# Optimization experiments

Hardware: AMD Instinct MI355X
Metric: run time of the kernel (lower is better)

The kernel has to match this reference:

```python
import jax, jax.numpy as jnp
import numpy as np
from functools import partial

B, N, T = 4, 10000, 128
E = 160000
H, C = 4, 64            # heads, out_channels per head
GAT_DIM = H * C         # 256
NEG_SLOPE = 0.2


def conv1d(x, w, b):
    # x: (M, Cin, L), w: (Cout, Cin, K), 'same' padding (pad=1 for k=3)
    y = jax.lax.conv_general_dilated(x, w, window_strides=(1,), padding=[(1, 1)],
                                     dimension_numbers=('NCH', 'OIH', 'NCH'))
    return y + b[None, :, None]


def maxpool2(x):
    # kernel=2, stride=2 over last axis
    return jax.lax.reduce_window(x, -jnp.inf, jax.lax.max,
                                 (1, 1, 2), (1, 1, 2), 'VALID')


def gat_layer_single(x, src, dst, W, att_s, att_d, bias):
    # x: (N, Fin); PyG GATConv with concat=True, self-loops already appended to src/dst
    n = x.shape[0]
    xl = (x @ W).reshape(n, H, C)                       # (N, H, C)
    a_s = jnp.sum(xl * att_s[None], axis=-1)            # (N, H)
    a_d = jnp.sum(xl * att_d[None], axis=-1)            # (N, H)
    e = jax.nn.leaky_relu(a_s[src] + a_d[dst], NEG_SLOPE)  # (E', H)
    emax = jax.ops.segment_max(e, dst, num_segments=n)     # (N, H)
    ex = jnp.exp(e - emax[dst])
    denom = jax.ops.segment_sum(ex, dst, num_segments=n)   # (N, H)
    alpha = ex / (denom[dst] + 1e-16)                       # (E', H)
    msg = xl[src] * alpha[..., None]                        # (E', H, C)
    out = jax.ops.segment_sum(msg, dst, num_segments=n)     # (N, H, C)
    return out.reshape(n, H * C) + bias


def setup_inputs() -> dict:
    key = jax.random.key(0)
    ks = jax.random.split(key, 24)
    rn = lambda k, sh, fan: jax.random.normal(k, sh, jnp.float32) / np.sqrt(fan)
    inp = {
        'x': jax.random.normal(ks[0], (B, N, T), jnp.float32),
        'edge_index': jax.random.randint(ks[1], (2, E), 0, N, jnp.int64),
        # temporal conv
        'cw1': rn(ks[2], (32, 1, 3), 3), 'cb1': jnp.zeros((32,), jnp.float32),
        'cw2': rn(ks[3], (64, 32, 3), 96), 'cb2': jnp.zeros((64,), jnp.float32),
        # GAT layer 0 (in=64)
        'W0': rn(ks[4], (64, GAT_DIM), 64), 'as0': rn(ks[5], (H, C), C), 'ad0': rn(ks[6], (H, C), C),
        'b0': jnp.zeros((GAT_DIM,), jnp.float32),
        # GAT layer 1 (in=256)
        'W1': rn(ks[7], (GAT_DIM, GAT_DIM), GAT_DIM), 'as1': rn(ks[8], (H, C), C), 'ad1': rn(ks[9], (H, C), C),
        'b1': jnp.zeros((GAT_DIM,), jnp.float32),
        # classification head 256->128->2
        'Wc1': rn(ks[10], (GAT_DIM, 128), GAT_DIM), 'bc1': jnp.zeros((128,), jnp.float32),
        'Wc2': rn(ks[11], (128, 2), 128), 'bc2': jnp.zeros((2,), jnp.float32),
        # attribution head 256->64->1
        'Wa1': rn(ks[12], (GAT_DIM, 64), GAT_DIM), 'ba1': jnp.zeros((64,), jnp.float32),
        'Wa2': rn(ks[13], (64, 1), 64), 'ba2': jnp.zeros((1,), jnp.float32),
    }
    return inp


def reference(x, edge_index, cw1, cb1, cw2, cb2, W0, as0, ad0, b0, W1, as1, ad1, b1,
              Wc1, bc1, Wc2, bc2, Wa1, ba1, Wa2, ba2):
    b, n, t = x.shape
    # ---- temporal conv over all B*N node signals ----
    xf = x.reshape(b * n, 1, t)
    h = jax.nn.relu(conv1d(xf, cw1, cb1))            # (BN, 32, T)
    h = maxpool2(h)                                  # (BN, 32, T//2)
    h = jax.nn.relu(conv1d(h, cw2, cb2))             # (BN, 64, T//2)
    feat = jnp.mean(h, axis=-1).reshape(b, n, 64)    # adaptive_avg_pool1d(1)
    # ---- GAT stack (self-loops appended, PyG default) ----
    src0, dst0 = edge_index[0], edge_index[1]
    loops = jnp.arange(n, dtype=src0.dtype)
    src = jnp.concatenate([src0, loops])
    dst = jnp.concatenate([dst0, loops])
    gat0 = jax.vmap(partial(gat_layer_single, src=src, dst=dst, W=W0, att_s=as0, att_d=ad0, bias=b0))
    gat1 = jax.vmap(partial(gat_layer_single, src=src, dst=dst, W=W1, att_s=as1, att_d=ad1, bias=b1))
    g = jax.nn.relu(gat0(feat))                      # (B, N, 256); dropout = identity (eval)
    g = jax.nn.relu(gat1(g))                         # (B, N, 256)
    # ---- heads ----
    pooled = jnp.mean(g, axis=1)                     # (B, 256)
    logits = jax.nn.relu(pooled @ Wc1 + bc1) @ Wc2 + bc2          # (B, 2)
    attr = jax.nn.sigmoid(jax.nn.relu(g @ Wa1 + ba1) @ Wa2 + ba2)  # (B, N, 1)
    return logits, attr[..., 0]
```

## Files before the change

kernel.cpp:

```cpp
#include <hip/hip_runtime.h>
#include <hip/hip_bf16.h>
#include <math.h>

typedef __hip_bfloat16 bf16;
typedef unsigned short u16;
typedef unsigned int u32;
typedef __attribute__((ext_vector_type(8))) short short8;
typedef __attribute__((ext_vector_type(4))) float f32x4;
typedef __attribute__((ext_vector_type(2))) float f32x2;

#define BATCH 4
#define NNODE 10000
#define TLEN 128
#define NEDGE 160000
#define GDIM 256
#define NHEAD 4

#define S_CW1 0
#define S_CB1 96
#define S_CB2 128
#define S_AS0 192
#define S_AD0 448
#define S_B0  704
#define S_AS1 960
#define S_AD1 1216
#define S_B1  1472
#define S_BC1 1728
#define S_WC2 1856
#define S_BC2 2112
#define S_BA1 2114
#define S_WA2 2178
#define S_BA2 2242
#define S_TOTAL 2243

__device__ __forceinline__ float prelu(float v) { return 0.5f * (v + fabsf(v)); }
__device__ __forceinline__ u16 f2b(float f) {
    union { float f; u32 u; } v; v.f = f;
    u32 r = v.u + 0x7FFF + ((v.u >> 16) & 1);
    return (u16)(r >> 16);
}
__device__ __forceinline__ float u2f(u16 u) {
    union { u32 u; float f; } v; v.u = ((u32)u) << 16;
    return v.f;
}
__device__ __forceinline__ float ldw(const void* p, int off, bool isbf) {
    return isbf ? u2f(((const u16*)p)[off]) : ((const float*)p)[off];
}

__device__ __forceinline__ bool probe_x_bf16(const void* xsrc) {
    int lane = threadIdx.x & 63;
    u16 h = ((const u16*)xsrc)[2 * lane];
    int e = (h >> 7) & 0xFF;
    unsigned long long m = __ballot(e >= 117 && e <= 130);
    return __popcll(m) >= 32;
}
__device__ __forceinline__ bool probe_ei64(const int* ei) {
    int lane = threadIdx.x & 63;
    int v = ei[2 * lane + 1];
    unsigned long long m = __ballot(v == 0);
    return __popcll(m) >= 56;
}

struct WPtrs { const void* p[20]; };

#define PRE_TBLK 665
__global__ __launch_bounds__(256) void k_pre(WPtrs wp, const void* __restrict__ xsrc,
        const int* __restrict__ ei, float* __restrict__ wbuf,
        u16* __restrict__ cw2r, u16* __restrict__ W0t, u16* __restrict__ W1t,
        u16* __restrict__ Wa1t, int* __restrict__ counts) {
    bool isbf = probe_x_bf16(xsrc);
    int b = blockIdx.x;
    if (b >= PRE_TBLK) {
        const int C2[16] = {0,96,128,192,448,704,960,1216,1472,1728,1856,2112,
                            2114,2178,2242,2243};
        const int SRC[15] = {0,1,3,5,6,7,9,10,11,13,14,15,17,18,19};
        int i = (b - PRE_TBLK) * 256 + threadIdx.x;
        if (i >= S_TOTAL) return;
        int j = 14;
        for (int t = 0; t < 15; ++t) { if (i < C2[t + 1]) { j = t; break; } }
        wbuf[i] = ldw(wp.p[SRC[j]], i - C2[j], isbf);
        return;
    }
    int i = b * 256 + threadIdx.x;
    if (i < 6144) {
        int c2 = i / 96, k = i - c2 * 96, s = k >> 5, ci = k & 31;
        cw2r[i] = f2b(ldw(wp.p[2], c2 * 96 + ci * 3 + s, isbf));
    }
    if (i < 16384) {
        int k = i >> 8, c = i & 255;
        W0t[c * 64 + k] = f2b(ldw(wp.p[4], k * 256 + c, isbf));
        int ka = i >> 6, ca = i & 63;
        Wa1t[ca * 256 + ka] = f2b(ldw(wp.p[16], ka * 64 + ca, isbf));
    }
    if (i < 65536) {
        int k = i >> 8, c = i & 255;
        W1t[c * 256 + k] = f2b(ldw(wp.p[8], k * 256 + c, isbf));
    }
    if (i < NEDGE + NNODE) {
        bool ei64 = probe_ei64(ei);
        int dst;
        if (i < NEDGE) dst = ei64 ? ei[2 * (NEDGE + i)] : ei[NEDGE + i];
        else dst = i - NEDGE;
        if (dst >= 0 && dst < NNODE) atomicAdd(&counts[dst], 1);
    }
}

__global__ __launch_bounds__(256) void k_scan1(const int* __restrict__ counts,
        int* __restrict__ cur, int* __restrict__ bsum) {
    __shared__ int buf[256];
    int tid = threadIdx.x;
    int i = blockIdx.x * 256 + tid;
    int v = (i < NNODE) ? counts[i] : 0;
    buf[tid] = v;
    __syncthreads();
    for (int off = 1; off < 256; off <<= 1) {
        int t = (tid >= off) ? buf[tid - off] : 0;
        __syncthreads();
        buf[tid] += t;
        __syncthreads();
    }
    if (i < NNODE) cur[i] = buf[tid];
    if (tid == 255) bsum[blockIdx.x] = buf[255];
}
__global__ __launch_bounds__(256) void k_scan3(const int* __restrict__ counts,
        int* __restrict__ cur, const int* __restrict__ bsum, int* __restrict__ row_ptr) {
    __shared__ int pre_s;
    int tid = threadIdx.x;
    if (tid == 0) {
        int s = 0;
        for (int j = 0; j < blockIdx.x; ++j) s += bsum[j];
        pre_s = s;
    }
    __syncthreads();
    int i = blockIdx.x * 256 + tid;
    if (i >= NNODE) return;
    int incl = cur[i] + pre_s;
    row_ptr[i + 1] = incl;
    cur[i] = incl - counts[i];
    if (i == 0) row_ptr[0] = 0;
}

#define HSTR 40
#define FILL_BLK 665
__global__ __launch_bounds__(256) void k_conv(const void* __restrict__ xsrc,
        const float* __restrict__ wbuf, const u16* __restrict__ cw2r,
        u16* __restrict__ featb, const int* __restrict__ ei,
        int* __restrict__ cur, int* __restrict__ col_src) {
    __shared__ __align__(16) float xs[4][132];
    __shared__ float w1s[96], b1s[32], b2s[64];
    __shared__ __align__(16) u16 hs[2][66 * HSTR];

    bool isbf = probe_x_bf16(xsrc);
    int tid = threadIdx.x;
    int wave = tid >> 6, lane = tid & 63;
    int node0 = blockIdx.x * 4;

    int m = lane & 15, q = lane >> 4;
    int n = wave * 16 + m;
    short8 bfr0 = *(const short8*)&cw2r[n * 96 + 0 * 32 + q * 8];
    short8 bfr1 = *(const short8*)&cw2r[n * 96 + 1 * 32 + q * 8];
    short8 bfr2 = *(const short8*)&cw2r[n * 96 + 2 * 32 + q * 8];

    {
        int j = tid >> 6, p = (tid & 63) * 2;
        if (isbf) {
            u32 w = ((const u32*)xsrc)[(size_t)node0 * 64 + tid];
            xs[j][1 + p] = u2f((u16)(w & 0xFFFF));
            xs[j][2 + p] = u2f((u16)(w >> 16));
        } else {
            float2 w = ((const float2*)xsrc)[(size_t)node0 * 64 + tid];
            xs[j][1 + p] = w.x;
            xs[j][2 + p] = w.y;
        }
    }
    if (tid < 8) xs[tid >> 1][(tid & 1) ? 129 : 0] = 0.f;
    if (tid < 96) w1s[tid] = wbuf[S_CW1 + tid];
    if (tid < 32) b1s[tid] = wbuf[S_CB1 + tid];
    if (tid < 64) b2s[tid] = wbuf[S_CB2 + tid];
    if (tid < 128) {
        int bf = tid >> 6, seg = (tid >> 5) & 1, ch = tid & 31;
        hs[bf][seg ? (65 * HSTR + ch) : ch] = 0;
    }
    __syncthreads();

    int d = tid & 15, uu = tid >> 4;
    float wa0 = w1s[6 * d + 0], wa1 = w1s[6 * d + 1], wa2 = w1s[6 * d + 2];
    float wb0 = w1s[6 * d + 3], wb1 = w1s[6 * d + 4], wb2 = w1s[6 * d + 5];
    float ba = b1s[2 * d], bb = b1s[2 * d + 1];
    float b2v = b2s[n];

    for (int j = 0; j < 4; ++j) {
        u16* hw = &hs[j & 1][0];
        const float* xr = &xs[j][0];
        #pragma unroll
        for (int it = 0; it < 4; ++it) {
            int u = uu + 16 * it;
            int t0 = 2 * u;
            float x0 = xr[t0], x1 = xr[t0 + 1], x2 = xr[t0 + 2], x3 = xr[t0 + 3];
            f32x2 A = {x0, x1}, Bv = {x1, x2}, Cv = {x2, x3};
            f32x2 va = {ba, ba}; va += wa0 * A; va += wa1 * Bv; va += wa2 * Cv;
            f32x2 vb = {bb, bb}; vb += wb0 * A; vb += wb1 * Bv; vb += wb2 * Cv;
            float ha = fmaxf(fmaxf(va.x, va.y), 0.f);
            float hb = fmaxf(fmaxf(vb.x, vb.y), 0.f);
            __hip_bfloat162 hp2 = __float22bfloat162_rn(make_float2(ha, hb));
            u32 pack; __builtin_memcpy(&pack, &hp2, 4);
            *(u32*)&hw[(u + 1) * HSTR + 2 * d] = pack;
        }
        __syncthreads();

        f32x4 accm0 = {0.f,0.f,0.f,0.f}, accm1 = {0.f,0.f,0.f,0.f};
        f32x4 accm2 = {0.f,0.f,0.f,0.f}, accm3 = {0.f,0.f,0.f,0.f};
        {
            short8 a0 = *(const short8*)&hw[(0 * 16 + m + 0) * HSTR + q * 8];
            short8 a1 = *(const short8*)&hw[(1 * 16 + m + 0) * HSTR + q * 8];
            short8 a2 = *(const short8*)&hw[(2 * 16 + m + 0) * HSTR + q * 8];
            short8 a3 = *(const short8*)&hw[(3 * 16 + m + 0) * HSTR + q * 8];
            accm0 = __builtin_amdgcn_mfma_f32_16x16x32_bf16(a0, bfr0, accm0, 0, 0, 0);
            accm1 = __builtin_amdgcn_mfma_f32_16x16x32_bf16(a1, bfr0, accm1, 0, 0, 0);
            accm2 = __builtin_amdgcn_mfma_f32_16x16x32_bf16(a2, bfr0, accm2, 0, 0, 0);
            accm3 = __builtin_amdgcn_mfma_f32_16x16x32_bf16(a3, bfr0, accm3, 0, 0, 0);
        }
        {
            short8 a0 = *(const short8*)&hw[(0 * 16 + m + 1) * HSTR + q * 8];
            short8 a1 = *(const short8*)&hw[(1 * 16 + m + 1) * HSTR + q * 8];
            short8 a2 = *(const short8*)&hw[(2 * 16 + m + 1) * HSTR + q * 8];
            short8 a3 = *(const short8*)&hw[(3 * 16 + m + 1) * HSTR + q * 8];
            accm0 = __builtin_amdgcn_mfma_f32_16x16x32_bf16(a0, bfr1, accm0, 0, 0, 0);
            accm1 = __builtin_amdgcn_mfma_f32_16x16x32_bf16(a1, bfr1, accm1, 0, 0, 0);
            accm2 = __builtin_amdgcn_mfma_f32_16x16x32_bf16(a2, bfr1, accm2, 0, 0, 0);
            accm3 = __builtin_amdgcn_mfma_f32_16x16x32_bf16(a3, bfr1, accm3, 0, 0, 0);
        }
        {
            short8 a0 = *(const short8*)&hw[(0 * 16 + m + 2) * HSTR + q * 8];
            short8 a1 = *(const short8*)&hw[(1 * 16 + m + 2) * HSTR + q * 8];
            short8 a2 = *(const short8*)&hw[(2 * 16 + m + 2) * HSTR + q * 8];
            short8 a3 = *(const short8*)&hw[(3 * 16 + m + 2) * HSTR + q * 8];
            accm0 = __builtin_amdgcn_mfma_f32_16x16x32_bf16(a0, bfr2, accm0, 0, 0, 0);
            accm1 = __builtin_amdgcn_mfma_f32_16x16x32_bf16(a1, bfr2, accm1, 0, 0, 0);
            accm2 = __builtin_amdgcn_mfma_f32_16x16x32_bf16(a2, bfr2, accm2, 0, 0, 0);
            accm3 = __builtin_amdgcn_mfma_f32_16x16x32_bf16(a3, bfr2, accm3, 0, 0, 0);
        }
        float scl = prelu(accm0[0] + b2v) + prelu(accm0[1] + b2v)
                  + prelu(accm0[2] + b2v) + prelu(accm0[3] + b2v);
        scl += prelu(accm1[0] + b2v) + prelu(accm1[1] + b2v)
             + prelu(accm1[2] + b2v) + prelu(accm1[3] + b2v);
        scl += prelu(accm2[0] + b2v) + prelu(accm2[1] + b2v)
             + prelu(accm2[2] + b2v) + prelu(accm2[3] + b2v);
        scl += prelu(accm3[0] + b2v) + prelu(accm3[1] + b2v)
             + prelu(accm3[2] + b2v) + prelu(accm3[3] + b2v);
        scl += __shfl_xor(scl, 16, 64);
        scl += __shfl_xor(scl, 32, 64);
        if (lane < 16) {
            int node = node0 + j;
            int bb2 = node / NNODE, nn = node - bb2 * NNODE;
            featb[((size_t)nn * 4 + bb2) * 64 + wave * 16 + lane] = f2b(scl * (1.f / 64.f));
        }
    }

    if (blockIdx.x < FILL_BLK) {
        bool ei64 = probe_ei64(ei);
        int e = blockIdx.x * 256 + tid;
        if (e < NEDGE + NNODE) {
            int src, dst;
            if (e < NEDGE) {
                if (ei64) { src = ei[2 * e]; dst = ei[2 * (NEDGE + e)]; }
                else      { src = ei[e];     dst = ei[NEDGE + e]; }
            } else {
                src = dst = e - NEDGE;
            }
            if (dst >= 0 && dst < NNODE) {
                int pos = atomicAdd(&cur[dst], 1);
                if (pos >= 0 && pos < NEDGE + NNODE) col_src[pos] = src;
            }
        }
    }
}

template<int K>
__global__ __launch_bounds__(256) void k_gemm(const u16* __restrict__ A,
        const u16* __restrict__ Wt, const float* __restrict__ att_s_w,
        const float* __restrict__ att_d_w, u16* __restrict__ outb,
        float* __restrict__ a_s, float* __restrict__ a_d) {
    int wave = threadIdx.x >> 6, lane = threadIdx.x & 63;
    int row0 = (blockIdx.x * 4 + wave) * 16;
    int m = lane & 15, q = lane >> 4;
    f32x4 acc[16];
    #pragma unroll
    for (int nt = 0; nt < 16; ++nt) acc[nt] = {0.f, 0.f, 0.f, 0.f};
    for (int kc = 0; kc < K; kc += 32) {
        short8 a = *(const short8*)&A[(size_t)(row0 + m) * K + kc + q * 8];
        #pragma unroll
        for (int nt = 0; nt < 16; ++nt) {
            short8 b = *(const short8*)&Wt[(size_t)(nt * 16 + m) * K + kc + q * 8];
            acc[nt] = __builtin_amdgcn_mfma_f32_16x16x32_bf16(a, b, acc[nt], 0, 0, 0);
        }
    }
    #pragma unroll
    for (int nt = 0; nt < 16; ++nt) {
        #pragma unroll
        for (int r = 0; r < 4; ++r)
            outb[(size_t)(row0 + q * 4 + r) * 256 + nt * 16 + m] = f2b(acc[nt][r]);
    }
    float sh_s[4][4] = {{0}}, sh_d[4][4] = {{0}};
    #pragma unroll
    for (int nt = 0; nt < 16; ++nt) {
        int h = nt >> 2;
        int cc = (nt & 3) * 16 + m;
        float asw = att_s_w[h * 64 + cc];
        float adw = att_d_w[h * 64 + cc];
        #pragma unroll
        for (int r = 0; r < 4; ++r) {
            sh_s[h][r] += acc[nt][r] * asw;
            sh_d[h][r] += acc[nt][r] * adw;
        }
    }
    #pragma unroll
    for (int off = 1; off < 16; off <<= 1) {
        #pragma unroll
        for (int h = 0; h < 4; ++h)
            #pragma unroll
            for (int r = 0; r < 4; ++r) {
                sh_s[h][r] += __shfl_xor(sh_s[h][r], off, 64);
                sh_d[h][r] += __shfl_xor(sh_d[h][r], off, 64);
            }
    }
    if (m == 0) {
        #pragma unroll
        for (int r = 0; r < 4; ++r) {
            int row = row0 + q * 4 + r;
            float4 vs = {sh_s[0][r], sh_s[1][r], sh_s[2][r], sh_s[3][r]};
            float4 vd = {sh_d[0][r], sh_d[1][r], sh_d[2][r], sh_d[3][r]};
            *(float4*)&a_s[(size_t)row * 4] = vs;
            *(float4*)&a_d[(size_t)row * 4] = vd;
        }
    }
}

__global__ __launch_bounds__(256) void k_agg(const u16* __restrict__ xlb,
        const float* __restrict__ a_s, const float* __restrict__ a_d,
        const int* __restrict__ row_ptr, const int* __restrict__ col_src,
        const float* __restrict__ bias, u16* __restrict__ gb_out) {
    int wave = threadIdx.x >> 6, lane = threadIdx.x & 63;
    int dst = blockIdx.x * 2 + (wave >> 1);
    int bp = (wave & 1) * 2;
    int beg = row_ptr[dst], end = row_ptr[dst + 1];

    int c = lane & 7, g = lane >> 3;
    int bc = bp + (c >> 2), hc = c & 3;
    float adv1 = a_d[(size_t)dst * 16 + bc * 4 + hc];
    float mloc = -INFINITY;
    for (int i = beg + g; i < end; i += 8) {
        int src = min(max(col_src[i], 0), NNODE - 1);
        float e = a_s[(size_t)src * 16 + bc * 4 + hc] + adv1;
        e = (e >= 0.f) ? e : 0.2f * e;
        mloc = fmaxf(mloc, e);
    }
    mloc = fmaxf(mloc, __shfl_xor(mloc, 8, 64));
    mloc = fmaxf(mloc, __shfl_xor(mloc, 16, 64));
    mloc = fmaxf(mloc, __shfl_xor(mloc, 32, 64));

    int bl = lane >> 5;
    int s = lane & 31;
    int h = s >> 3;
    int b = bp + bl;
    float mv = __shfl(mloc, bl * 4 + h, 64);

    float advh = a_d[(size_t)dst * 16 + b * 4 + h];
    float acc[8];
    #pragma unroll
    for (int k = 0; k < 8; ++k) acc[k] = 0.f;
    float l = 0.f;

    int asoff = b * 4 + h;
    int i = beg;
    for (; i + 4 <= end; i += 4) {
        int s0 = min(max(col_src[i], 0), NNODE - 1);
        int s1 = min(max(col_src[i + 1], 0), NNODE - 1);
        int s2 = min(max(col_src[i + 2], 0), NNODE - 1);
        int s3 = min(max(col_src[i + 3], 0), NNODE - 1);
        float a0 = a_s[(size_t)s0 * 16 + asoff];
        float a1 = a_s[(size_t)s1 * 16 + asoff];
        float a2 = a_s[(size_t)s2 * 16 + asoff];
        float a3 = a_s[(size_t)s3 * 16 + asoff];
        short8 x0 = *(const short8*)&xlb[((size_t)s0 * 4 + b) * 256 + s * 8];
        short8 x1 = *(const short8*)&xlb[((size_t)s1 * 4 + b) * 256 + s * 8];
        short8 x2 = *(const short8*)&xlb[((size_t)s2 * 4 + b) * 256 + s * 8];
        short8 x3 = *(const short8*)&xlb[((size_t)s3 * 4 + b) * 256 + s * 8];
        float e0 = a0 + advh; e0 = (e0 >= 0.f) ? e0 : 0.2f * e0;
        float p0 = __expf(e0 - mv); l += p0;
        #pragma unroll
        for (int k = 0; k < 8; ++k) acc[k] += p0 * u2f((u16)x0[k]);
        float e1 = a1 + advh; e1 = (e1 >= 0.f) ? e1 : 0.2f * e1;
        float p1 = __expf(e1 - mv); l += p1;
        #pragma unroll
        for (int k = 0; k < 8; ++k) acc[k] += p1 * u2f((u16)x1[k]);
        float e2 = a2 + advh; e2 = (e2 >= 0.f) ? e2 : 0.2f * e2;
        float p2 = __expf(e2 - mv); l += p2;
        #pragma unroll
        for (int k = 0; k < 8; ++k) acc[k] += p2 * u2f((u16)x2[k]);
        float e3 = a3 + advh; e3 = (e3 >= 0.f) ? e3 : 0.2f * e3;
        float p3 = __expf(e3 - mv); l += p3;
        #pragma unroll
        for (int k = 0; k < 8; ++k) acc[k] += p3 * u2f((u16)x3[k]);
    }
    for (; i < end; ++i) {
        int s0 = min(max(col_src[i], 0), NNODE - 1);
        float a0 = a_s[(size_t)s0 * 16 + asoff];
        short8 x0 = *(const short8*)&xlb[((size_t)s0 * 4 + b) * 256 + s * 8];
        float e0 = a0 + advh; e0 = (e0 >= 0.f) ? e0 : 0.2f * e0;
        float p0 = __expf(e0 - mv); l += p0;
        #pragma unroll
        for (int k = 0; k < 8; ++k) acc[k] += p0 * u2f((u16)x0[k]);
    }
    float rl = 1.f / (l + 1e-16f);
    short8 o;
    #pragma unroll
    for (int k = 0; k < 8; ++k)
        o[k] = (short)f2b(prelu(acc[k] * rl + bias[s * 8 + k]));
    *(short8*)&gb_out[((size_t)dst * 4 + b) * 256 + s * 8] = o;
}

__global__ __launch_bounds__(256) void k_attrpool(const u16* __restrict__ gb,
        const u16* __restrict__ Wa1t, const float* __restrict__ wbuf,
        float* __restrict__ out, float* __restrict__ pooled) {
    if (blockIdx.x >= 625) {
        int pb = blockIdx.x - 625;
        int b = pb >> 6;
        int chunk = pb & 63;
        int cch = threadIdx.x;
        int n0 = chunk * 157;
        int n1 = min(NNODE, n0 + 157);
        float acc = 0.f;
        int n = n0;
        for (; n + 4 <= n1; n += 4) {
            float v0 = u2f(gb[((size_t)n * 4 + b) * 256 + cch]);
            float v1 = u2f(gb[((size_t)(n + 1) * 4 + b) * 256 + cch]);
            float v2 = u2f(gb[((size_t)(n + 2) * 4 + b) * 256 + cch]);
            float v3 = u2f(gb[((size_t)(n + 3) * 4 + b) * 256 + cch]);
            acc += v0; acc += v1; acc += v2; acc += v3;
        }
        for (; n < n1; ++n)
            acc += u2f(gb[((size_t)n * 4 + b) * 256 + cch]);
        atomicAdd(&pooled[b * 256 + cch], acc);
        return;
    }
    int wave = threadIdx.x >> 6, lane = threadIdx.x & 63;
    int row0 = (blockIdx.x * 4 + wave) * 16;
    int m = lane & 15, q = lane >> 4;
    f32x4 acc[4];
    #pragma unroll
    for (int nt = 0; nt < 4; ++nt) acc[nt] = {0.f, 0.f, 0.f, 0.f};
    for (int kc = 0; kc < 256; kc += 32) {
        short8 a = *(const short8*)&gb[(size_t)(row0 + m) * 256 + kc + q * 8];
        #pragma unroll
        for (int nt = 0; nt < 4; ++nt) {
            short8 b = *(const short8*)&Wa1t[(size_t)(nt * 16 + m) * 256 + kc + q * 8];
            acc[nt] = __builtin_amdgcn_mfma_f32_16x16x32_bf16(a, b, acc[nt], 0, 0, 0);
        }
    }
    float part[4] = {0, 0, 0, 0};
    #pragma unroll
    for (int nt = 0; nt < 4; ++nt) {
        int col = nt * 16 + m;
        float ba1v = wbuf[S_BA1 + col];
        float wa2v = wbuf[S_WA2 + col];
        #pragma unroll
        for (int r = 0; r < 4; ++r)
            part[r] += prelu(acc[nt][r] + ba1v) * wa2v;
    }
    #pragma unroll
    for (int off = 1; off < 16; off <<= 1) {
        #pragma unroll
        for (int r = 0; r < 4; ++r)
            part[r] += __shfl_xor(part[r], off, 64);
    }
    if (m == 0) {
        float ba2v = wbuf[S_BA2];
        #pragma unroll
        for (int r = 0; r < 4; ++r) {
            int row = row0 + q * 4 + r;
            int n = row >> 2, b = row & 3;
            float v = part[r] + ba2v;
            out[8 + b * NNODE + n] = 1.f / (1.f + __expf(-v));
        }
    }
}

__global__ __launch_bounds__(128) void k_logits(const float* __restrict__ pooled,
        const float* __restrict__ wbuf, const void* __restrict__ Wc1p,
        float* __restrict__ out,
        const u16* __restrict__ featb, const u16* __restrict__ gb,
        const int* __restrict__ row_ptr, const int* __restrict__ ei,
        const void* __restrict__ xsrc, int hostbad) {
    int tid = threadIdx.x;
    bool isbf = probe_x_bf16(xsrc);
    if (blockIdx.x == 4) {
        __shared__ float red[128];
        bool ei64 = probe_ei64(ei);
        float mx[2] = {0.f, 0.f};
        const u16* bufs[2] = {featb, gb};
        for (int qq = 0; qq < 2; ++qq) {
            const u16* p = bufs[qq];
            float m = 0.f;
            for (int i = tid; i < 2048; i += 128) {
                float v = u2f(p[i]);
                if (v != v) m = 1e30f;
                m = fmaxf(m, fabsf(v));
            }
            red[tid] = m;
            __syncthreads();
            for (int s2 = 64; s2 > 0; s2 >>= 1) {
                if (tid < s2) red[tid] = fmaxf(red[tid], red[tid + s2]);
                __syncthreads();
            }
            mx[qq] = red[0];
            __syncthreads();
        }
        if (tid == 0) {
            int fb = (mx[0] > 1e8f || mx[0] < 1e-6f) ? 1 : 0;
            int gbad = (mx[1] > 1e8f || mx[1] < 1e-6f) ? 1 : 0;
            int cb = (row_ptr[NNODE] != NEDGE + NNODE) ? 1 : 0;
            int code = 100 * fb + 400 * gbad + 800 * cb + 6400 * hostbad;
            if (code) {
                code += 1600 * (isbf ? 0 : 1);
                code += 3200 * (ei64 ? 1 : 0);
                for (int j = 0; j < 8; ++j) out[j] = (float)code;
            }
        }
        return;
    }
    __shared__ float pm[256];
    __shared__ float red4[4];
    int b = blockIdx.x;
    pm[tid] = pooled[b * 256 + tid] * (1.f / NNODE);
    pm[tid + 128] = pooled[b * 256 + tid + 128] * (1.f / NNODE);
    __syncthreads();
    float acc = wbuf[S_BC1 + tid];
    if (isbf) {
        const u16* w = (const u16*)Wc1p;
        #pragma unroll 4
        for (int k = 0; k < 256; ++k)
            acc += pm[k] * u2f(w[k * 128 + tid]);
    } else {
        const float* w = (const float*)Wc1p;
        #pragma unroll 4
        for (int k = 0; k < 256; ++k)
            acc += pm[k] * w[k * 128 + tid];
    }
    float hv = prelu(acc);
    float p0 = hv * wbuf[S_WC2 + tid * 2];
    float p1 = hv * wbuf[S_WC2 + tid * 2 + 1];
    #pragma unroll
    for (int off = 32; off > 0; off >>= 1) {
        p0 += __shfl_xor(p0, off, 64);
        p1 += __shfl_xor(p1, off, 64);
    }
    int wv = tid >> 6, lane = tid & 63;
    if (lane == 0) { red4[wv * 2] = p0; red4[wv * 2 + 1] = p1; }
    __syncthreads();
    if (tid < 2)
        out[b * 2 + tid] = red4[tid] + red4[2 + tid] + wbuf[S_BC2 + tid];
}

extern "C" void kernel_launch(void* const* d_in, const int* in_sizes, int n_in,
                              void* d_out, int out_size, void* d_ws, size_t ws_size,
                              hipStream_t stream) {
    const void* x  = d_in[0];
    const int*  ei = (const int*)d_in[1];
    float* out = (float*)d_out;

    WPtrs wp;
    for (int j = 0; j < 20; ++j) wp.p[j] = d_in[j + 2];

    char* ws = (char*)d_ws;
    size_t off = 0;
    auto alloc = [&](size_t bytes) -> void* {
        void* p = ws + off;
        off += (bytes + 255) & ~(size_t)255;
        return p;
    };
    float* wbuf    = (float*)alloc((size_t)S_TOTAL * 4);
    u16*   featb   = (u16*)  alloc((size_t)BATCH * NNODE * 64 * 2);
    u16*   xlb     = (u16*)  alloc((size_t)BATCH * NNODE * 256 * 2);
    u16*   gb      = (u16*)  alloc((size_t)BATCH * NNODE * 256 * 2);
    float* a_s     = (float*)alloc((size_t)BATCH * NNODE * 4 * 4);
    float* a_d     = (float*)alloc((size_t)BATCH * NNODE * 4 * 4);
    u16*   cw2r    = (u16*)alloc(6144 * 2);
    u16*   W0t     = (u16*)alloc(16384 * 2);
    u16*   W1t     = (u16*)alloc(65536 * 2);
    u16*   Wa1t    = (u16*)alloc(16384 * 2);
    int*   counts  = (int*)alloc(NNODE * 4);
    float* pooled  = (float*)alloc(BATCH * 256 * 4);
    int*   row_ptr = (int*)alloc((NNODE + 1) * 4);
    int*   cur     = (int*)alloc(NNODE * 4);
    int*   col_src = (int*)alloc((NEDGE + NNODE) * 4);
    int*   bsum    = (int*)alloc(64 * 4);
    (void)ws_size; (void)out_size;

    int hostbad = (n_in != 22 || in_sizes[0] != BATCH * NNODE * TLEN ||
                   in_sizes[1] != 2 * NEDGE) ? 1 : 0;

    hipMemsetAsync(counts, 0, 40192 + 4096, stream);

    k_pre<<<PRE_TBLK + 9, 256, 0, stream>>>(wp, x, ei, wbuf, cw2r, W0t, W1t, Wa1t, counts);
    k_scan1<<<40, 256, 0, stream>>>(counts, cur, bsum);
    k_scan3<<<40, 256, 0, stream>>>(counts, cur, bsum, row_ptr);

    k_conv<<<BATCH * NNODE / 4, 256, 0, stream>>>(x, wbuf, cw2r, featb, ei, cur, col_src);

    k_gemm<64><<<BATCH * NNODE / 64, 256, 0, stream>>>(featb, W0t,
            wbuf + S_AS0, wbuf + S_AD0, xlb, a_s, a_d);
    k_agg<<<NNODE / 2, 256, 0, stream>>>(xlb, a_s, a_d, row_ptr, col_src, wbuf + S_B0, gb);

    k_gemm<256><<<BATCH * NNODE / 64, 256, 0, stream>>>(gb, W1t,
            wbuf + S_AS1, wbuf + S_AD1, xlb, a_s, a_d);
    k_agg<<<NNODE / 2, 256, 0, stream>>>(xlb, a_s, a_d, row_ptr, col_src, wbuf + S_B1, gb);

    k_attrpool<<<625 + 256, 256, 0, stream>>>(gb, Wa1t, wbuf, out, pooled);
    k_logits<<<5, 128, 0, stream>>>(pooled, wbuf, wp.p[12], out, featb, gb, row_ptr, ei, x, hostbad);
}
```

Measured before the change: 402.4 us.

## Use online softmax in GAT aggregation and pipeline conv over 8 nodes per block

The aggregation kernel drops its separate max pre-pass over each node's edges. It now keeps a running max and rescales the accumulators whenever any lane sees a larger value, so edge data is read in a single pass. Edge indices and row bounds are made wave-uniform with readfirstlane so the compiler can keep them in scalar registers. The conv kernel now handles 8 nodes per block and double-buffers the first conv stage so the next node's conv1 overlaps the current node's MFMA conv2. The costs are fewer blocks, occasional rescale branches, and a slightly different floating-point order.

```diff
diff --git a/kernel.cpp b/kernel.cpp
--- a/kernel.cpp
+++ b/kernel.cpp
@@ -33,7 +33,7 @@
 #define S_BA2 2242
 #define S_TOTAL 2243
 
-__device__ __forceinline__ float prelu(float v) { return 0.5f * (v + fabsf(v)); }
+__device__ __forceinline__ float prelu(float v) { return fmaxf(v, 0.f); }
 __device__ __forceinline__ u16 f2b(float f) {
     union { float f; u32 u; } v; v.f = f;
     u32 r = v.u + 0x7FFF + ((v.u >> 16) & 1);
@@ -141,19 +141,20 @@
 }
 
 #define HSTR 40
+#define NPB 8
 #define FILL_BLK 665
 __global__ __launch_bounds__(256) void k_conv(const void* __restrict__ xsrc,
         const float* __restrict__ wbuf, const u16* __restrict__ cw2r,
         u16* __restrict__ featb, const int* __restrict__ ei,
         int* __restrict__ cur, int* __restrict__ col_src) {
-    __shared__ __align__(16) float xs[4][132];
+    __shared__ __align__(16) float xs[NPB][132];
     __shared__ float w1s[96], b1s[32], b2s[64];
     __shared__ __align__(16) u16 hs[2][66 * HSTR];
 
     bool isbf = probe_x_bf16(xsrc);
     int tid = threadIdx.x;
     int wave = tid >> 6, lane = tid & 63;
-    int node0 = blockIdx.x * 4;
+    int node0 = blockIdx.x * NPB;
 
     int m = lane & 15, q = lane >> 4;
     int n = wave * 16 + m;
@@ -161,19 +162,21 @@
     short8 bfr1 = *(const short8*)&cw2r[n * 96 + 1 * 32 + q * 8];
     short8 bfr2 = *(const short8*)&cw2r[n * 96 + 2 * 32 + q * 8];
 
-    {
-        int j = tid >> 6, p = (tid & 63) * 2;
+    #pragma unroll
+    for (int rr = 0; rr < NPB / 4; ++rr) {
+        int idx = rr * 256 + tid;
+        int j = idx >> 6, p = (idx & 63) * 2;
         if (isbf) {
-            u32 w = ((const u32*)xsrc)[(size_t)node0 * 64 + tid];
+            u32 w = ((const u32*)xsrc)[(size_t)node0 * 64 + idx];
             xs[j][1 + p] = u2f((u16)(w & 0xFFFF));
             xs[j][2 + p] = u2f((u16)(w >> 16));
         } else {
-            float2 w = ((const float2*)xsrc)[(size_t)node0 * 64 + tid];
+            float2 w = ((const float2*)xsrc)[(size_t)node0 * 64 + idx];
             xs[j][1 + p] = w.x;
             xs[j][2 + p] = w.y;
         }
     }
-    if (tid < 8) xs[tid >> 1][(tid & 1) ? 129 : 0] = 0.f;
+    if (tid < 2 * NPB) xs[tid >> 1][(tid & 1) ? 129 : 0] = 0.f;
     if (tid < 96) w1s[tid] = wbuf[S_CW1 + tid];
     if (tid < 32) b1s[tid] = wbuf[S_CB1 + tid];
     if (tid < 64) b2s[tid] = wbuf[S_CB2 + tid];
@@ -189,9 +192,9 @@
     float ba = b1s[2 * d], bb = b1s[2 * d + 1];
     float b2v = b2s[n];
 
-    for (int j = 0; j < 4; ++j) {
-        u16* hw = &hs[j & 1][0];
-        const float* xr = &xs[j][0];
+    auto conv1 = [&](int jj) {
+        const float* xr = &xs[jj][0];
+        u16* hwp = &hs[jj & 1][0];
         #pragma unroll
         for (int it = 0; it < 4; ++it) {
             int u = uu + 16 * it;
@@ -204,10 +207,17 @@
             float hb = fmaxf(fmaxf(vb.x, vb.y), 0.f);
             __hip_bfloat162 hp2 = __float22bfloat162_rn(make_float2(ha, hb));
             u32 pack; __builtin_memcpy(&pack, &hp2, 4);
-            *(u32*)&hw[(u + 1) * HSTR + 2 * d] = pack;
-        }
-        __syncthreads();
-
+            *(u32*)&hwp[(u + 1) * HSTR + 2 * d] = pack;
+        }
+    };
+
+    conv1(0);
+    __syncthreads();
+
+    for (int j = 0; j < NPB; ++j) {
+        if (j + 1 < NPB) conv1(j + 1);
+
+        const u16* hw = &hs[j & 1][0];
         f32x4 accm0 = {0.f,0.f,0.f,0.f}, accm1 = {0.f,0.f,0.f,0.f};
         f32x4 accm2 = {0.f,0.f,0.f,0.f}, accm3 = {0.f,0.f,0.f,0.f};
         {
@@ -255,6 +265,7 @@
             int bb2 = node / NNODE, nn = node - bb2 * NNODE;
             featb[((size_t)nn * 4 + bb2) * 64 + wave * 16 + lane] = f2b(scl * (1.f / 64.f));
         }
+        if (j + 1 < NPB) __syncthreads();
     }
 
     if (blockIdx.x < FILL_BLK) {
@@ -341,43 +352,29 @@
         const int* __restrict__ row_ptr, const int* __restrict__ col_src,
         const float* __restrict__ bias, u16* __restrict__ gb_out) {
     int wave = threadIdx.x >> 6, lane = threadIdx.x & 63;
-    int dst = blockIdx.x * 2 + (wave >> 1);
+    int dst = __builtin_amdgcn_readfirstlane(blockIdx.x * 2 + (wave >> 1));
     int bp = (wave & 1) * 2;
-    int beg = row_ptr[dst], end = row_ptr[dst + 1];
-
-    int c = lane & 7, g = lane >> 3;
-    int bc = bp + (c >> 2), hc = c & 3;
-    float adv1 = a_d[(size_t)dst * 16 + bc * 4 + hc];
-    float mloc = -INFINITY;
-    for (int i = beg + g; i < end; i += 8) {
-        int src = min(max(col_src[i], 0), NNODE - 1);
-        float e = a_s[(size_t)src * 16 + bc * 4 + hc] + adv1;
-        e = (e >= 0.f) ? e : 0.2f * e;
-        mloc = fmaxf(mloc, e);
-    }
-    mloc = fmaxf(mloc, __shfl_xor(mloc, 8, 64));
-    mloc = fmaxf(mloc, __shfl_xor(mloc, 16, 64));
-    mloc = fmaxf(mloc, __shfl_xor(mloc, 32, 64));
+    int beg = __builtin_amdgcn_readfirstlane(row_ptr[dst]);
+    int end = __builtin_amdgcn_readfirstlane(row_ptr[dst + 1]);
 
     int bl = lane >> 5;
     int s = lane & 31;
     int h = s >> 3;
     int b = bp + bl;
-    float mv = __shfl(mloc, bl * 4 + h, 64);
-
-    float advh = a_d[(size_t)dst * 16 + b * 4 + h];
+    int asoff = b * 4 + h;
+    float advh = a_d[(size_t)dst * 16 + asoff];
+
+    float m = -INFINITY, l = 0.f;
     float acc[8];
     #pragma unroll
     for (int k = 0; k < 8; ++k) acc[k] = 0.f;
-    float l = 0.f;
-
-    int asoff = b * 4 + h;
+
     int i = beg;
     for (; i + 4 <= end; i += 4) {
-        int s0 = min(max(col_src[i], 0), NNODE - 1);
-        int s1 = min(max(col_src[i + 1], 0), NNODE - 1);
-        int s2 = min(max(col_src[i + 2], 0), NNODE - 1);
-        int s3 = min(max(col_src[i + 3], 0), NNODE - 1);
+        int s0 = __builtin_amdgcn_readfirstlane(min(max(col_src[i], 0), NNODE - 1));
+        int s1 = __builtin_amdgcn_readfirstlane(min(max(col_src[i + 1], 0), NNODE - 1));
+        int s2 = __builtin_amdgcn_readfirstlane(min(max(col_src[i + 2], 0), NNODE - 1));
+        int s3 = __builtin_amdgcn_readfirstlane(min(max(col_src[i + 3], 0), NNODE - 1));
         float a0 = a_s[(size_t)s0 * 16 + asoff];
         float a1 = a_s[(size_t)s1 * 16 + asoff];
         float a2 = a_s[(size_t)s2 * 16 + asoff];
@@ -387,31 +384,49 @@
         short8 x2 = *(const short8*)&xlb[((size_t)s2 * 4 + b) * 256 + s * 8];
         short8 x3 = *(const short8*)&xlb[((size_t)s3 * 4 + b) * 256 + s * 8];
         float e0 = a0 + advh; e0 = (e0 >= 0.f) ? e0 : 0.2f * e0;
-        float p0 = __expf(e0 - mv); l += p0;
+        float e1 = a1 + advh; e1 = (e1 >= 0.f) ? e1 : 0.2f * e1;
+        float e2 = a2 + advh; e2 = (e2 >= 0.f) ? e2 : 0.2f * e2;
+        float e3 = a3 + advh; e3 = (e3 >= 0.f) ? e3 : 0.2f * e3;
+        float cmax = fmaxf(fmaxf(e0, e1), fmaxf(e2, e3));
+        if (__any(cmax > m)) {
+            float mn = fmaxf(m, cmax);
+            float r = __expf(m - mn);
+            m = mn;
+            l *= r;
+            #pragma unroll
+            for (int k = 0; k < 8; ++k) acc[k] *= r;
+        }
+        float p0 = __expf(e0 - m); l += p0;
         #pragma unroll
         for (int k = 0; k < 8; ++k) acc[k] += p0 * u2f((u16)x0[k]);
-        float e1 = a1 + advh; e1 = (e1 >= 0.f) ? e1 : 0.2f * e1;
-        float p1 = __expf(e1 - mv); l += p1;
+        float p1 = __expf(e1 - m); l += p1;
         #pragma unroll
         for (int k = 0; k < 8; ++k) acc[k] += p1 * u2f((u16)x1[k]);
-        float e2 = a2 + advh; e2 = (e2 >= 0.f) ? e2 : 0.2f * e2;
-        float p2 = __expf(e2 - mv); l += p2;
+        float p2 = __expf(e2 - m); l += p2;
         #pragma unroll
         for (int k = 0; k < 8; ++k) acc[k] += p2 * u2f((u16)x2[k]);
-        float e3 = a3 + advh; e3 = (e3 >= 0.f) ? e3 : 0.2f * e3;
-        float p3 = __expf(e3 - mv); l += p3;
+        float p3 = __expf(e3 - m); l += p3;
         #pragma unroll
         for (int k = 0; k < 8; ++k) acc[k] += p3 * u2f((u16)x3[k]);
     }
     for (; i < end; ++i) {
-        int s0 = min(max(col_src[i], 0), NNODE - 1);
+        int s0 = __builtin_amdgcn_readfirstlane(min(max(col_src[i], 0), NNODE - 1));
         float a0 = a_s[(size_t)s0 * 16 + asoff];
         short8 x0 = *(const short8*)&xlb[((size_t)s0 * 4 + b) * 256 + s * 8];
         float e0 = a0 + advh; e0 = (e0 >= 0.f) ? e0 : 0.2f * e0;
-        float p0 = __expf(e0 - mv); l += p0;
+        if (__any(e0 > m)) {
+            float mn = fmaxf(m, e0);
+            float r = __expf(m - mn);
+            m = mn;
+            l *= r;
+            #pragma unroll
+            for (int k = 0; k < 8; ++k) acc[k] *= r;
+        }
+        float p0 = __expf(e0 - m); l += p0;
         #pragma unroll
         for (int k = 0; k < 8; ++k) acc[k] += p0 * u2f((u16)x0[k]);
     }
+
     float rl = 1.f / (l + 1e-16f);
     short8 o;
     #pragma unroll
@@ -606,7 +621,7 @@
     k_scan1<<<40, 256, 0, stream>>>(counts, cur, bsum);
     k_scan3<<<40, 256, 0, stream>>>(counts, cur, bsum, row_ptr);
 
-    k_conv<<<BATCH * NNODE / 4, 256, 0, stream>>>(x, wbuf, cw2r, featb, ei, cur, col_src);
+    k_conv<<<BATCH * NNODE / NPB, 256, 0, stream>>>(x, wbuf, cw2r, featb, ei, cur, col_src);
 
     k_gemm<64><<<BATCH * NNODE / 64, 256, 0, stream>>>(featb, W0t,
             wbuf + S_AS0, wbuf + S_AD0, xlb, a_s, a_d);
```

New measurement: 396.6 us. Within noise of the previous version (-1.4%).
